# Kernel tuning notes

Measured on AMD Instinct MI355X. Metric: run time of the kernel, lower is better.

The kernel has to match this reference:

```python
import jax, jax.numpy as jnp
import numpy as np

N, E, C = 50000, 300000, 128


def _line_graph(src, dst, n):
    # PyG LineGraph(force_directed=True): line-graph node per edge; edge j -> edge i iff dst(j) == src(i)
    order = np.argsort(src, kind='stable')          # edges grouped by src node
    deg_out = np.bincount(src, minlength=n)
    ptr = np.concatenate([np.zeros(1, np.int64), np.cumsum(deg_out)])
    counts = deg_out[dst]                           # #successor edges of each edge j
    total = int(counts.sum())
    line_src = np.repeat(np.arange(src.shape[0], dtype=np.int64), counts)
    grp_start = np.repeat(ptr[dst], counts)
    cum = np.cumsum(counts)
    within = np.arange(total, dtype=np.int64) - np.repeat(cum - counts, counts)
    line_dst = order[grp_start + within]
    return np.stack([line_src, line_dst]).astype(np.int32)


def setup_inputs() -> dict:
    rng = np.random.default_rng(0)
    ei = rng.integers(0, N, size=(2, E), dtype=np.int64)
    line_ei = _line_graph(ei[0], ei[1], N)
    key = jax.random.key(0)
    k = jax.random.split(key, 6)
    s_e = float(1.0 / np.sqrt(3 * C))  # torch Linear init bound
    s_g = float(1.0 / np.sqrt(C))
    return {
        "x": jax.random.normal(k[0], (N, C), jnp.float32),
        "edge_attr": jax.random.normal(k[1], (E, C), jnp.float32),
        "W_edge": jax.random.uniform(k[2], (3 * C, C), jnp.float32, -s_e, s_e),
        "b_edge": jax.random.uniform(k[3], (C,), jnp.float32, -s_e, s_e),
        "W_gcn": jax.random.uniform(k[4], (C, C), jnp.float32, -s_g, s_g),
        "b_gcn": jnp.zeros((C,), jnp.float32),
        "edge_index": jnp.asarray(ei, dtype=jnp.int32),
        "batch": jnp.zeros((N,), jnp.int32),
        "line_edge_index": jnp.asarray(line_ei),
    }


def reference(x, edge_attr, W_edge, b_edge, W_gcn, b_gcn,
              edge_index, batch, line_edge_index):
    src, dst = edge_index[0], edge_index[1]
    # gather endpoints, concat with edge_attr, linear 3C -> C
    merged = jnp.concatenate([x[src], x[dst], edge_attr], axis=1)    # [E, 3C]
    line_x = merged @ W_edge + b_edge                                # [E, C] line-graph node feats

    # GCNConv with self loops on the line graph (line-graph nodes = original edges)
    e = line_x.shape[0]
    loops = jnp.arange(e, dtype=line_edge_index.dtype)
    row = jnp.concatenate([line_edge_index[0], loops])
    col = jnp.concatenate([line_edge_index[1], loops])
    xw = line_x @ W_gcn                                              # [E, C]
    deg = jax.ops.segment_sum(jnp.ones(row.shape, xw.dtype), col, num_segments=e)
    dinv = jnp.where(deg > 0, jax.lax.rsqrt(deg), 0.0)
    norm = dinv[row] * dinv[col]                                     # [M+E]
    out = jax.ops.segment_sum(xw[row] * norm[:, None], col, num_segments=e) + b_gcn
    return jax.nn.leaky_relu(out)  # negative_slope = 0.01 (torch default)
```

## Files before the change

kernel.cpp:

```cpp
#include <hip/hip_runtime.h>
#include <hip/hip_bf16.h>


typedef __bf16 bf16x8 __attribute__((ext_vector_type(8)));
typedef float  f32x4  __attribute__((ext_vector_type(4)));

#define C_DIM 128

__device__ __forceinline__ float bfu_lo(unsigned u) { return __uint_as_float(u << 16); }
__device__ __forceinline__ float bfu_hi(unsigned u) { return __uint_as_float(u & 0xffff0000u); }
__device__ __forceinline__ unsigned bf16_bits(float f) {
    __bf16 h = (__bf16)f;
    return (unsigned)__builtin_bit_cast(unsigned short, h);
}

__global__ void k_wcomb_indeg(const float* __restrict__ W_edge, const float* __restrict__ W_gcn,
                              const float* __restrict__ b_edge,
                              __bf16* __restrict__ Wf, float* __restrict__ b_comb,
                              const int* __restrict__ dst, int E, int* __restrict__ indeg) {
    if ((int)blockIdx.x < 192) {
        int idx = blockIdx.x * 256 + threadIdx.x;
        if (idx < 384 * 128) {
            int k = idx >> 7, c = idx & 127;
            float s = 0.f;
            for (int m = 0; m < 128; ++m) s += W_edge[k * 128 + m] * W_gcn[m * 128 + c];
            int ks = k >> 5, kc8 = (k >> 3) & 3, j = k & 7;
            int col16 = c >> 4, c15 = c & 15;
            Wf[(size_t)(((ks * 8 + col16) * 64) + kc8 * 16 + c15) * 8 + j] = (__bf16)s;
        }
        if (blockIdx.x == 0 && threadIdx.x < 128) {
            int c = threadIdx.x;
            float s = 0.f;
            for (int m = 0; m < 128; ++m) s += b_edge[m] * W_gcn[m * 128 + c];
            b_comb[c] = s;
        }
        return;
    }
    int e = ((int)blockIdx.x - 192) * 256 + threadIdx.x;
    if (e < E) atomicAdd(&indeg[dst[e]], 1);
}

__global__ void k_scan_bsum(const int* __restrict__ indeg, int n, int* __restrict__ bsum) {
    __shared__ int ws[16];
    int i = blockIdx.x * 1024 + threadIdx.x;
    int v = (i < n) ? indeg[i] : 0;
    int lane = threadIdx.x & 63, wid = threadIdx.x >> 6;
    for (int off = 32; off; off >>= 1) v += __shfl_down(v, off);
    if (lane == 0) ws[wid] = v;
    __syncthreads();
    if (threadIdx.x < 16) {
        int s = ws[threadIdx.x];
        for (int off = 8; off; off >>= 1) s += __shfl_down(s, off);
        if (threadIdx.x == 0) bsum[blockIdx.x] = s;
    }
}

__global__ void k_scan_fin(const int* __restrict__ indeg, int n, const int* __restrict__ bsum,
                           int nb, int* __restrict__ ptr, int* __restrict__ cursor) {
    __shared__ int wsum[16];
    __shared__ int s_boff, s_total;
    int lane = threadIdx.x & 63, wid = threadIdx.x >> 6;
    if (threadIdx.x < 64) {
        int v = (lane < nb) ? bsum[lane] : 0;
        int incl = v;
        for (int off = 1; off < 64; off <<= 1) {
            int t = __shfl_up(incl, off);
            if (lane >= off) incl += t;
        }
        if (lane == (int)blockIdx.x) s_boff = incl - v;
        if (lane == 63) s_total = incl;
    }
    int i = blockIdx.x * 1024 + threadIdx.x;
    int v = (i < n) ? indeg[i] : 0;
    int incl = v;
    for (int off = 1; off < 64; off <<= 1) {
        int t = __shfl_up(incl, off);
        if (lane >= off) incl += t;
    }
    if (lane == 63) wsum[wid] = incl;
    __syncthreads();
    if (wid == 0 && lane < 16) {
        int s = wsum[lane];
        for (int off = 1; off < 16; off <<= 1) {
            int t = __shfl_up(s, off);
            if (lane >= off) s += t;
        }
        wsum[lane] = s;
    }
    __syncthreads();
    int woff = wid ? wsum[wid - 1] : 0;
    if (i < n) {
        int ex = s_boff + woff + incl - v;
        ptr[i] = ex;
        cursor[i] = ex;
    }
    if (blockIdx.x == 0 && threadIdx.x == 0) ptr[n] = s_total;
}

__global__ __launch_bounds__(256) void k_place_p12(
    const int* __restrict__ dst, int E, int nbPlace,
    int* __restrict__ cursor, int* __restrict__ adj,
    const float* __restrict__ x, const __bf16* __restrict__ Wf,
    const float* __restrict__ b_comb,
    __bf16* __restrict__ P1, __bf16* __restrict__ P2, int M) {

    __shared__ __align__(16) __bf16 As[64 * 136];

    if ((int)blockIdx.x < nbPlace) {
        int e = blockIdx.x * 256 + threadIdx.x;
        if (e < E) {
            int pos = atomicAdd(&cursor[dst[e]], 1);
            adj[pos] = e;
        }
        return;
    }

    const int tid = threadIdx.x;
    const int mbase = ((int)blockIdx.x - nbPlace) * 64;
    const int r = tid >> 2, q = tid & 3;
    const int m_r = mbase + r;
    const int m_rc = (m_r < M) ? m_r : 0;
    const float* rp = x + (size_t)m_rc * C_DIM;

#pragma unroll
    for (int s4 = 0; s4 < 4; ++s4) {
        const float* p = rp + s4 * 32 + q * 8;
        float4 f0 = *(const float4*)p;
        float4 f1 = *(const float4*)(p + 4);
        bf16x8 h;
        h[0] = (__bf16)f0.x; h[1] = (__bf16)f0.y; h[2] = (__bf16)f0.z; h[3] = (__bf16)f0.w;
        h[4] = (__bf16)f1.x; h[5] = (__bf16)f1.y; h[6] = (__bf16)f1.z; h[7] = (__bf16)f1.w;
        int u = s4 * 4 + q;
        *(bf16x8*)&As[r * 128 + ((u ^ (r & 7)) << 3)] = h;
    }
    __syncthreads();

    const int lane = tid & 63, wid = tid >> 6;
    const int wr = wid >> 1, wc = wid & 1;
    const int kc8 = lane >> 4;
    const int arow0 = wr * 32 + (lane & 15);
    const int arow1 = arow0 + 16;
    const __bf16* wfb = Wf + ((size_t)(wc * 4) * 64 + lane) * 8;

    f32x4 acc1[2][4] = {};
    f32x4 acc2[2][4] = {};

#pragma unroll
    for (int ks = 0; ks < 4; ++ks) {
        int u = ks * 4 + kc8;
        bf16x8 a0 = *(const bf16x8*)&As[arow0 * 128 + ((u ^ (arow0 & 7)) << 3)];
        bf16x8 a1 = *(const bf16x8*)&As[arow1 * 128 + ((u ^ (arow1 & 7)) << 3)];
#pragma unroll
        for (int n = 0; n < 4; ++n) {
            bf16x8 b1 = *(const bf16x8*)&wfb[(size_t)(ks * 8 + n) * 64 * 8];
            bf16x8 b2 = *(const bf16x8*)&wfb[(size_t)((ks + 4) * 8 + n) * 64 * 8];
            acc1[0][n] = __builtin_amdgcn_mfma_f32_16x16x32_bf16(a0, b1, acc1[0][n], 0, 0, 0);
            acc1[1][n] = __builtin_amdgcn_mfma_f32_16x16x32_bf16(a1, b1, acc1[1][n], 0, 0, 0);
            acc2[0][n] = __builtin_amdgcn_mfma_f32_16x16x32_bf16(a0, b2, acc2[0][n], 0, 0, 0);
            acc2[1][n] = __builtin_amdgcn_mfma_f32_16x16x32_bf16(a1, b2, acc2[1][n], 0, 0, 0);
        }
    }

#pragma unroll
    for (int pass = 0; pass < 2; ++pass) {
        __syncthreads();
#pragma unroll
        for (int m = 0; m < 2; ++m)
#pragma unroll
            for (int j = 0; j < 4; ++j) {
                int row = wr * 32 + m * 16 + (lane >> 4) * 4 + j;
#pragma unroll
                for (int n = 0; n < 4; ++n) {
                    int c = wc * 64 + n * 16 + (lane & 15);
                    int p = ((c >> 2) & 3) * 32 + (c >> 4) * 4 + (c & 3);
                    float v = pass == 0 ? acc1[m][n][j] + b_comb[c] : acc2[m][n][j];
                    As[row * 136 + p] = (__bf16)v;
                }
            }
        __syncthreads();
        if (m_r < M) {
            __bf16* outp = (pass == 0 ? P1 : P2) + (size_t)m_r * C_DIM + q * 32;
#pragma unroll
            for (int i = 0; i < 4; ++i)
                *(bf16x8*)(outp + i * 8) = *(const bf16x8*)&As[r * 136 + q * 32 + i * 8];
        }
    }
}

__global__ __launch_bounds__(256) void k_gemm3(
    const float* __restrict__ ea, const __bf16* __restrict__ Wf,
    const __bf16* __restrict__ P1, const __bf16* __restrict__ P2,
    const int* __restrict__ src, const int* __restrict__ dst,
    const int* __restrict__ indeg, __bf16* __restrict__ xws, int E) {

    __shared__ __align__(16) __bf16 Wlds[16384];

    const int tid = threadIdx.x;
    {
        const uint4* wsrc = (const uint4*)Wf + 4096;
        uint4* wdst = (uint4*)Wlds;
#pragma unroll
        for (int i = 0; i < 8; ++i) wdst[tid + i * 256] = wsrc[tid + i * 256];
    }
    __syncthreads();

    const int wid = tid >> 6, lane = tid & 63;
    const int e15 = lane & 15, q = lane >> 4;
    const int eb0 = blockIdx.x * 128 + wid * 32;
    const int eb1 = eb0 + 16;
    if (eb0 >= E) return;
    const bool has1 = (eb1 < E);

    const int e0 = eb0 + e15;
    const int e0c = (e0 < E) ? e0 : E - 1;
    const int e1 = eb1 + e15;
    const int e1c = (e1 < E) ? e1 : E - 1;

    const int s0 = src[e0c], d0 = dst[e0c];
    const float di0 = rsqrtf(1.0f + (float)indeg[s0]);
    int s1 = s0, d1 = d0;
    float di1 = di0;
    if (has1) { s1 = src[e1c]; d1 = dst[e1c]; di1 = rsqrtf(1.0f + (float)indeg[s1]); }

    const float* ap0 = ea + (size_t)e0c * C_DIM + q * 8;
    float4 fa[8];
#pragma unroll
    for (int ks = 0; ks < 4; ++ks) {
        fa[2 * ks]     = *(const float4*)(ap0 + ks * 32);
        fa[2 * ks + 1] = *(const float4*)(ap0 + ks * 32 + 4);
    }
    uint4 hA1[4], hA2[4];
    {
        const uint4* p1 = (const uint4*)(P1 + (size_t)s0 * C_DIM + q * 32);
        const uint4* p2 = (const uint4*)(P2 + (size_t)d0 * C_DIM + q * 32);
#pragma unroll
        for (int m = 0; m < 4; ++m) { hA1[m] = p1[m]; hA2[m] = p2[m]; }
    }
    const float* ap1 = ea + (size_t)e1c * C_DIM + q * 8;
    float4 fb[8];
    if (has1) {
#pragma unroll
        for (int ks = 0; ks < 4; ++ks) {
            fb[2 * ks]     = *(const float4*)(ap1 + ks * 32);
            fb[2 * ks + 1] = *(const float4*)(ap1 + ks * 32 + 4);
        }
    }

    f32x4 acc[8] = {};
#pragma unroll
    for (int ks = 0; ks < 4; ++ks) {
        float4 f0 = fa[2 * ks], f1 = fa[2 * ks + 1];
        bf16x8 b;
        b[0] = (__bf16)f0.x; b[1] = (__bf16)f0.y; b[2] = (__bf16)f0.z; b[3] = (__bf16)f0.w;
        b[4] = (__bf16)f1.x; b[5] = (__bf16)f1.y; b[6] = (__bf16)f1.z; b[7] = (__bf16)f1.w;
#pragma unroll
        for (int n = 0; n < 8; ++n) {
            bf16x8 a = *(const bf16x8*)&Wlds[(size_t)((ks * 8 + n) * 64 + lane) * 8];
            acc[n] = __builtin_amdgcn_mfma_f32_16x16x32_bf16(a, b, acc[n], 0, 0, 0);
        }
    }

    uint4 hB1[4], hB2[4];
    if (has1) {
        const uint4* p1 = (const uint4*)(P1 + (size_t)s1 * C_DIM + q * 32);
        const uint4* p2 = (const uint4*)(P2 + (size_t)d1 * C_DIM + q * 32);
#pragma unroll
        for (int m = 0; m < 4; ++m) { hB1[m] = p1[m]; hB2[m] = p2[m]; }
    }

    if (e0 < E) {
        __bf16* op = xws + (size_t)e0 * C_DIM + q * 32;
#pragma unroll
        for (int m = 0; m < 4; ++m) {
            bf16x8 h1 = __builtin_bit_cast(bf16x8, hA1[m]);
            bf16x8 h2 = __builtin_bit_cast(bf16x8, hA2[m]);
            uint4 u;
            unsigned w[4];
#pragma unroll
            for (int hw = 0; hw < 4; ++hw) {
                int n = 2 * m + (hw >> 1);
                int j0 = (hw & 1) * 2;
                float v0 = (acc[n][j0]     + (float)h1[(hw >> 1) * 4 + j0]     + (float)h2[(hw >> 1) * 4 + j0])     * di0;
                float v1 = (acc[n][j0 + 1] + (float)h1[(hw >> 1) * 4 + j0 + 1] + (float)h2[(hw >> 1) * 4 + j0 + 1]) * di0;
                w[hw] = bf16_bits(v0) | (bf16_bits(v1) << 16);
            }
            u.x = w[0]; u.y = w[1]; u.z = w[2]; u.w = w[3];
            *(uint4*)(op + m * 8) = u;
        }
    }

    if (!has1) return;

    f32x4 acc2[8] = {};
#pragma unroll
    for (int ks = 0; ks < 4; ++ks) {
        float4 f0 = fb[2 * ks], f1 = fb[2 * ks + 1];
        bf16x8 b;
        b[0] = (__bf16)f0.x; b[1] = (__bf16)f0.y; b[2] = (__bf16)f0.z; b[3] = (__bf16)f0.w;
        b[4] = (__bf16)f1.x; b[5] = (__bf16)f1.y; b[6] = (__bf16)f1.z; b[7] = (__bf16)f1.w;
#pragma unroll
        for (int n = 0; n < 8; ++n) {
            bf16x8 a = *(const bf16x8*)&Wlds[(size_t)((ks * 8 + n) * 64 + lane) * 8];
            acc2[n] = __builtin_amdgcn_mfma_f32_16x16x32_bf16(a, b, acc2[n], 0, 0, 0);
        }
    }

    if (e1 < E) {
        __bf16* op = xws + (size_t)e1 * C_DIM + q * 32;
#pragma unroll
        for (int m = 0; m < 4; ++m) {
            bf16x8 h1 = __builtin_bit_cast(bf16x8, hB1[m]);
            bf16x8 h2 = __builtin_bit_cast(bf16x8, hB2[m]);
            uint4 u;
            unsigned w[4];
#pragma unroll
            for (int hw = 0; hw < 4; ++hw) {
                int n = 2 * m + (hw >> 1);
                int j0 = (hw & 1) * 2;
                float v0 = (acc2[n][j0]     + (float)h1[(hw >> 1) * 4 + j0]     + (float)h2[(hw >> 1) * 4 + j0])     * di1;
                float v1 = (acc2[n][j0 + 1] + (float)h1[(hw >> 1) * 4 + j0 + 1] + (float)h2[(hw >> 1) * 4 + j0 + 1]) * di1;
                w[hw] = bf16_bits(v0) | (bf16_bits(v1) << 16);
            }
            u.x = w[0]; u.y = w[1]; u.z = w[2]; u.w = w[3];
            *(uint4*)(op + m * 8) = u;
        }
    }
}

__global__ void k_agg(const __bf16* __restrict__ xws, const int* __restrict__ ptr,
                      const int* __restrict__ adj, __bf16* __restrict__ agg, int Nn) {
    int v = blockIdx.x * 4 + (threadIdx.x >> 6);
    if (v >= Nn) return;
    int c = threadIdx.x & 63;
    int b0 = ptr[v], b1 = ptr[v + 1];
    float s0 = 0.f, s1 = 0.f;
    for (int t = b0; t < b1; ++t) {
        int j = adj[t];
        unsigned u = *(const unsigned*)(xws + (size_t)j * C_DIM + c * 2);
        s0 += bfu_lo(u);
        s1 += bfu_hi(u);
    }
    unsigned o = bf16_bits(s0) | (bf16_bits(s1) << 16);
    *(unsigned*)(agg + (size_t)v * C_DIM + c * 2) = o;
}

__global__ void k_out(const __bf16* __restrict__ xws, const __bf16* __restrict__ agg,
                      const int* __restrict__ src, const int* __restrict__ indeg,
                      const float* __restrict__ b_gcn, float* __restrict__ out, int E) {
    int g = blockIdx.x * 256 + threadIdx.x;
    if (g >= E * (C_DIM / 4)) return;
    int e = g >> 5, c4 = (g & 31) * 4;
    int p4 = ((c4 >> 2) & 3) * 32 + (c4 >> 4) * 4;
    int s = src[e];
    float di = rsqrtf(1.0f + (float)indeg[s]);
    uint2 u  = *(const uint2*)(xws + (size_t)e * C_DIM + p4);
    uint2 au = *(const uint2*)(agg + (size_t)s * C_DIM + p4);
    float4 b = *(const float4*)&b_gcn[c4];
    float4 r;
    r.x = di * (bfu_lo(au.x) + bfu_lo(u.x)) + b.x;
    r.y = di * (bfu_hi(au.x) + bfu_hi(u.x)) + b.y;
    r.z = di * (bfu_lo(au.y) + bfu_lo(u.y)) + b.z;
    r.w = di * (bfu_hi(au.y) + bfu_hi(u.y)) + b.w;
    r.x = r.x > 0.f ? r.x : 0.01f * r.x;
    r.y = r.y > 0.f ? r.y : 0.01f * r.y;
    r.z = r.z > 0.f ? r.z : 0.01f * r.z;
    r.w = r.w > 0.f ? r.w : 0.01f * r.w;
    *(float4*)&out[(size_t)e * C_DIM + c4] = r;
}

extern "C" void kernel_launch(void* const* d_in, const int* in_sizes, int n_in,
                              void* d_out, int out_size, void* d_ws, size_t ws_size,
                              hipStream_t stream) {
    const float* x      = (const float*)d_in[0];
    const float* ea     = (const float*)d_in[1];
    const float* W_edge = (const float*)d_in[2];
    const float* b_edge = (const float*)d_in[3];
    const float* W_gcn  = (const float*)d_in[4];
    const float* b_gcn  = (const float*)d_in[5];
    const int*   ei     = (const int*)d_in[6];

    const int C  = in_sizes[3];
    const int Nn = in_sizes[0] / C;
    const int E  = in_sizes[1] / C;
    const int* srcp = ei;
    const int* dstp = ei + E;

    char* ws = (char*)d_ws;
    size_t off = 0;
    auto alloc = [&](size_t bytes) { size_t o = off; off = (off + bytes + 255) & ~(size_t)255; return o; };
    __bf16* Wf     = (__bf16*)(ws + alloc((size_t)384 * 128 * sizeof(__bf16)));
    float*  b_comb = (float*)(ws + alloc(128 * sizeof(float)));
    int*    indeg  = (int*)(ws + alloc((size_t)Nn * sizeof(int)));
    int*    ptr    = (int*)(ws + alloc((size_t)(Nn + 1) * sizeof(int)));
    int*    cursor = (int*)(ws + alloc((size_t)Nn * sizeof(int)));
    int*    bsum   = (int*)(ws + alloc(64 * sizeof(int)));
    int*    adj    = (int*)(ws + alloc((size_t)E * sizeof(int)));
    __bf16* P1     = (__bf16*)(ws + alloc((size_t)Nn * C * sizeof(__bf16)));
    __bf16* P2     = (__bf16*)(ws + alloc((size_t)Nn * C * sizeof(__bf16)));
    __bf16* xws    = (__bf16*)(ws + alloc((size_t)E * C * sizeof(__bf16)));
    __bf16* agg    = (__bf16*)(ws + alloc((size_t)Nn * C * sizeof(__bf16)));

    const int nb = (Nn + 1023) / 1024;
    const int nbE = (E + 255) / 256;
    const int nbP = (Nn + 63) / 64;

    (void)hipMemsetAsync(indeg, 0, (size_t)Nn * sizeof(int), stream);
    k_wcomb_indeg<<<192 + nbE, 256, 0, stream>>>(W_edge, W_gcn, b_edge, Wf, b_comb, dstp, E, indeg);
    k_scan_bsum<<<nb, 1024, 0, stream>>>(indeg, Nn, bsum);
    k_scan_fin<<<nb, 1024, 0, stream>>>(indeg, Nn, bsum, nb, ptr, cursor);
    k_place_p12<<<nbE + nbP, 256, 0, stream>>>(dstp, E, nbE, cursor, adj, x, Wf, b_comb, P1, P2, Nn);
    k_gemm3<<<(E + 127) / 128, 256, 0, stream>>>(ea, Wf, P1, P2, srcp, dstp, indeg, xws, E);
    k_agg<<<(Nn + 3) / 4, 256, 0, stream>>>(xws, ptr, adj, agg, Nn);
    k_out<<<(E * (C / 4) + 255) / 256, 256, 0, stream>>>(xws, agg, srcp, indeg, b_gcn, (float*)d_out, E);
}
```

Before: 223.5 us.

## Read GEMM weights from global memory, unroll aggregation, widen output kernel

The edge GEMM kernel no longer stages its 32 KB weight slice into LDS with a block barrier. Each lane instead loads its MFMA weight fragments straight from global memory, relying on the cache, which also lowers LDS use and may raise occupancy. The aggregation loop is unrolled by two with separate accumulators to keep more gathers in flight. The output kernel now has each thread handle 8 channels instead of 4, halving the thread count and the redundant src/indeg loads. The trade-off is repeated global or L2 weight reads inside the MFMA loop in place of LDS reads.

After: 229.9 us. 1.03x slower.

```diff
diff --git a/kernel.cpp b/kernel.cpp
--- a/kernel.cpp
+++ b/kernel.cpp
@@ -193,17 +193,7 @@
     const int* __restrict__ src, const int* __restrict__ dst,
     const int* __restrict__ indeg, __bf16* __restrict__ xws, int E) {
 
-    __shared__ __align__(16) __bf16 Wlds[16384];
-
     const int tid = threadIdx.x;
-    {
-        const uint4* wsrc = (const uint4*)Wf + 4096;
-        uint4* wdst = (uint4*)Wlds;
-#pragma unroll
-        for (int i = 0; i < 8; ++i) wdst[tid + i * 256] = wsrc[tid + i * 256];
-    }
-    __syncthreads();
-
     const int wid = tid >> 6, lane = tid & 63;
     const int e15 = lane & 15, q = lane >> 4;
     const int eb0 = blockIdx.x * 128 + wid * 32;
@@ -216,6 +206,8 @@
     const int e1 = eb1 + e15;
     const int e1c = (e1 < E) ? e1 : E - 1;
 
+    const __bf16* wfl = Wf + 32768 + (size_t)lane * 8;
+
     const int s0 = src[e0c], d0 = dst[e0c];
     const float di0 = rsqrtf(1.0f + (float)indeg[s0]);
     int s1 = s0, d1 = d0;
@@ -255,7 +247,7 @@
         b[4] = (__bf16)f1.x; b[5] = (__bf16)f1.y; b[6] = (__bf16)f1.z; b[7] = (__bf16)f1.w;
 #pragma unroll
         for (int n = 0; n < 8; ++n) {
-            bf16x8 a = *(const bf16x8*)&Wlds[(size_t)((ks * 8 + n) * 64 + lane) * 8];
+            bf16x8 a = *(const bf16x8*)(wfl + (size_t)(ks * 8 + n) * 512);
             acc[n] = __builtin_amdgcn_mfma_f32_16x16x32_bf16(a, b, acc[n], 0, 0, 0);
         }
     }
@@ -300,7 +292,7 @@
         b[4] = (__bf16)f1.x; b[5] = (__bf16)f1.y; b[6] = (__bf16)f1.z; b[7] = (__bf16)f1.w;
 #pragma unroll
         for (int n = 0; n < 8; ++n) {
-            bf16x8 a = *(const bf16x8*)&Wlds[(size_t)((ks * 8 + n) * 64 + lane) * 8];
+            bf16x8 a = *(const bf16x8*)(wfl + (size_t)(ks * 8 + n) * 512);
             acc2[n] = __builtin_amdgcn_mfma_f32_16x16x32_bf16(a, b, acc2[n], 0, 0, 0);
         }
     }
@@ -333,13 +325,21 @@
     if (v >= Nn) return;
     int c = threadIdx.x & 63;
     int b0 = ptr[v], b1 = ptr[v + 1];
-    float s0 = 0.f, s1 = 0.f;
-    for (int t = b0; t < b1; ++t) {
+    float s0 = 0.f, s1 = 0.f, t0 = 0.f, t1 = 0.f;
+    int t = b0;
+    for (; t + 2 <= b1; t += 2) {
+        int j0 = adj[t], j1 = adj[t + 1];
+        unsigned u0 = *(const unsigned*)(xws + (size_t)j0 * C_DIM + c * 2);
+        unsigned u1 = *(const unsigned*)(xws + (size_t)j1 * C_DIM + c * 2);
+        s0 += bfu_lo(u0); s1 += bfu_hi(u0);
+        t0 += bfu_lo(u1); t1 += bfu_hi(u1);
+    }
+    if (t < b1) {
         int j = adj[t];
         unsigned u = *(const unsigned*)(xws + (size_t)j * C_DIM + c * 2);
-        s0 += bfu_lo(u);
-        s1 += bfu_hi(u);
-    }
+        s0 += bfu_lo(u); s1 += bfu_hi(u);
+    }
+    s0 += t0; s1 += t1;
     unsigned o = bf16_bits(s0) | (bf16_bits(s1) << 16);
     *(unsigned*)(agg + (size_t)v * C_DIM + c * 2) = o;
 }
@@ -348,24 +348,28 @@
                       const int* __restrict__ src, const int* __restrict__ indeg,
                       const float* __restrict__ b_gcn, float* __restrict__ out, int E) {
     int g = blockIdx.x * 256 + threadIdx.x;
-    if (g >= E * (C_DIM / 4)) return;
-    int e = g >> 5, c4 = (g & 31) * 4;
-    int p4 = ((c4 >> 2) & 3) * 32 + (c4 >> 4) * 4;
+    if (g >= E * 16) return;
+    int e = g >> 4, c8 = (g & 15) * 8;
     int s = src[e];
     float di = rsqrtf(1.0f + (float)indeg[s]);
-    uint2 u  = *(const uint2*)(xws + (size_t)e * C_DIM + p4);
-    uint2 au = *(const uint2*)(agg + (size_t)s * C_DIM + p4);
-    float4 b = *(const float4*)&b_gcn[c4];
-    float4 r;
-    r.x = di * (bfu_lo(au.x) + bfu_lo(u.x)) + b.x;
-    r.y = di * (bfu_hi(au.x) + bfu_hi(u.x)) + b.y;
-    r.z = di * (bfu_lo(au.y) + bfu_lo(u.y)) + b.z;
-    r.w = di * (bfu_hi(au.y) + bfu_hi(u.y)) + b.w;
-    r.x = r.x > 0.f ? r.x : 0.01f * r.x;
-    r.y = r.y > 0.f ? r.y : 0.01f * r.y;
-    r.z = r.z > 0.f ? r.z : 0.01f * r.z;
-    r.w = r.w > 0.f ? r.w : 0.01f * r.w;
-    *(float4*)&out[(size_t)e * C_DIM + c4] = r;
+    float4 r[2];
+#pragma unroll
+    for (int h = 0; h < 2; ++h) {
+        int c4 = c8 + h * 4;
+        int p4 = ((c4 >> 2) & 3) * 32 + (c4 >> 4) * 4;
+        uint2 u  = *(const uint2*)(xws + (size_t)e * C_DIM + p4);
+        uint2 au = *(const uint2*)(agg + (size_t)s * C_DIM + p4);
+        float4 b = *(const float4*)&b_gcn[c4];
+        r[h].x = di * (bfu_lo(au.x) + bfu_lo(u.x)) + b.x;
+        r[h].y = di * (bfu_hi(au.x) + bfu_hi(u.x)) + b.y;
+        r[h].z = di * (bfu_lo(au.y) + bfu_lo(u.y)) + b.z;
+        r[h].w = di * (bfu_hi(au.y) + bfu_hi(u.y)) + b.w;
+        r[h].x = r[h].x > 0.f ? r[h].x : 0.01f * r[h].x;
+        r[h].y = r[h].y > 0.f ? r[h].y : 0.01f * r[h].y;
+        r[h].z = r[h].z > 0.f ? r[h].z : 0.01f * r[h].z;
+        r[h].w = r[h].w > 0.f ? r[h].w : 0.01f * r[h].w;
+        *(float4*)&out[(size_t)e * C_DIM + c4] = r[h];
+    }
 }
 
 extern "C" void kernel_launch(void* const* d_in, const int* in_sizes, int n_in,
@@ -411,5 +415,5 @@
     k_place_p12<<<nbE + nbP, 256, 0, stream>>>(dstp, E, nbE, cursor, adj, x, Wf, b_comb, P1, P2, Nn);
     k_gemm3<<<(E + 127) / 128, 256, 0, stream>>>(ea, Wf, P1, P2, srcp, dstp, indeg, xws, E);
     k_agg<<<(Nn + 3) / 4, 256, 0, stream>>>(xws, ptr, adj, agg, Nn);
-    k_out<<<(E * (C / 4) + 255) / 256, 256, 0, stream>>>(xws, agg, srcp, indeg, b_gcn, (float*)d_out, E);
-}
+    k_out<<<(E * 16 + 255) / 256, 256, 0, stream>>>(xws, agg, srcp, indeg, b_gcn, (float*)d_out, E);
+}
```
